# Performance work log

Measured on AMD Instinct MI355X. Metric: run time of the kernel, lower is better.

Reference implementation:

```python
import jax, jax.numpy as jnp
import numpy as np

T, H, I, E, K, L, R = 1024, 1024, 1024, 8, 2, 4, 16
N = 2 * I  # gate_up dim


def setup_inputs() -> dict:
    key = jax.random.key(0)
    ks = jax.random.split(key, 12)
    tw = jax.random.uniform(ks[1], (T, K), dtype=jnp.float32) + 0.1
    tw = tw / tw.sum(axis=-1, keepdims=True)  # routing weights sum to 1
    return {
        "hidden_states": jax.random.normal(ks[0], (T, H), dtype=jnp.float32),
        "topk_weights": tw,
        "w13": jax.random.normal(ks[2], (E, N, H), dtype=jnp.float32) * (1.0 / np.sqrt(H)),
        "w2": jax.random.normal(ks[3], (E, H, I), dtype=jnp.float32) * (1.0 / np.sqrt(I)),
        "gate_up_lora_a": jax.random.normal(ks[4], (L, E, R, H), dtype=jnp.float32) * (1.0 / np.sqrt(H)),
        "gate_up_lora_b": jax.random.normal(ks[5], (L, E, N, R), dtype=jnp.float32) * (1.0 / np.sqrt(R)),
        "down_lora_a": jax.random.normal(ks[6], (L, E, R, I), dtype=jnp.float32) * (1.0 / np.sqrt(I)),
        "down_lora_b": jax.random.normal(ks[7], (L, E, H, R), dtype=jnp.float32) * (1.0 / np.sqrt(R)),
        "scalings": jax.random.uniform(ks[8], (L,), dtype=jnp.float32) + 0.5,
        "topk_ids": jax.random.randint(ks[9], (T, K), 0, E, dtype=jnp.int32),
        "lora_indices": jax.random.randint(ks[10], (T,), 0, L, dtype=jnp.int32),
    }


def reference(hidden_states, topk_weights, w13, w2, gate_up_lora_a,
              gate_up_lora_b, down_lora_a, down_lora_b, scalings,
              topk_ids, lora_indices):
    num_tokens, hidden = hidden_states.shape
    num_experts, gate_up_dim, _ = w13.shape
    top_k = topk_ids.shape[1]
    inter = gate_up_dim // 2
    TKp = num_tokens * top_k

    e_flat = topk_ids.reshape(-1)                      # [TK] expert per dispatched pair
    l_flat = jnp.repeat(lora_indices, top_k)           # [TK] adapter per pair
    w_flat = topk_weights.reshape(-1)                  # [TK] routing weight
    x_rep = jnp.repeat(hidden_states, top_k, axis=0)   # [TK, H]

    # ---- grouped gate_up GEMM (base path): cache1[p] = x[p] @ w13[e(p)]^T ----
    cache1 = jnp.zeros((TKp, gate_up_dim), dtype=hidden_states.dtype)
    for ei in range(num_experts):  # small fixed expert count
        mask = (e_flat == ei)[:, None]
        cache1 = cache1 + jnp.where(mask, x_rep @ w13[ei].T, 0.0)

    # ---- per-expert gate_up LoRA delta, injected BEFORE activation ----
    scal = scalings[l_flat][:, None]                   # [TK, 1]
    Ag = gate_up_lora_a[l_flat, e_flat]                # [TK, R, H]
    Bg = gate_up_lora_b[l_flat, e_flat]                # [TK, N, R]
    tmp = jnp.einsum('prh,ph->pr', Ag, x_rep)
    cache1 = cache1 + jnp.einsum('pnr,pr->pn', Bg, tmp) * scal

    # ---- silu_and_mul on (base + lora) ----
    act = jax.nn.silu(cache1[:, :inter]) * cache1[:, inter:]   # [TK, I]

    # ---- grouped down GEMM (base), routed-weight applied ----
    cache3 = jnp.zeros((TKp, hidden), dtype=hidden_states.dtype)
    for ei in range(num_experts):
        mask = (e_flat == ei)[:, None]
        cache3 = cache3 + jnp.where(mask, act @ w2[ei].T, 0.0)
    cache3 = cache3 * w_flat[:, None]

    # ---- per-expert down LoRA delta (weighted by routing weight) ----
    Ad = down_lora_a[l_flat, e_flat]                   # [TK, R, I]
    Bd = down_lora_b[l_flat, e_flat]                   # [TK, H, R]
    tmpd = jnp.einsum('pri,pi->pr', Ad, act)
    cache3 = cache3 + jnp.einsum('phr,pr->ph', Bd, tmpd) * scal * w_flat[:, None]

    # ---- combine expert outputs (moe_sum over top_k slots) ----
    return cache3.reshape(num_tokens, top_k, hidden).sum(axis=1)
```

## Files before the change

kernel.cpp:

```cpp
#include <hip/hip_runtime.h>
#include <stdint.h>

#define Td 1024
#define Hd 1024
#define Id 1024
#define Ed 8
#define Kd 2
#define Ld 4
#define Rd 16
#define Nd 2048
#define TKd (Td*Kd)

typedef __bf16 bf16x8 __attribute__((ext_vector_type(8)));
typedef float f32x4 __attribute__((ext_vector_type(4)));

__device__ __forceinline__ ushort f2bf(float f) {
    uint32_t u = __builtin_bit_cast(uint32_t, f);
    return (ushort)((u + 0x7fffu + ((u >> 16) & 1u)) >> 16);
}
__device__ __forceinline__ float bf2f(ushort u) {
    uint32_t x = ((uint32_t)u) << 16;
    return __builtin_bit_cast(float, x);
}
__device__ __forceinline__ void cvt16(const float* __restrict__ s, ushort* __restrict__ d) {
    float4 a0 = *(const float4*)(s);
    float4 a1 = *(const float4*)(s + 4);
    float4 a2 = *(const float4*)(s + 8);
    float4 a3 = *(const float4*)(s + 12);
    uint4 o0, o1;
    o0.x = (uint)f2bf(a0.x) | ((uint)f2bf(a0.y) << 16);
    o0.y = (uint)f2bf(a0.z) | ((uint)f2bf(a0.w) << 16);
    o0.z = (uint)f2bf(a1.x) | ((uint)f2bf(a1.y) << 16);
    o0.w = (uint)f2bf(a1.z) | ((uint)f2bf(a1.w) << 16);
    o1.x = (uint)f2bf(a2.x) | ((uint)f2bf(a2.y) << 16);
    o1.y = (uint)f2bf(a2.z) | ((uint)f2bf(a2.w) << 16);
    o1.z = (uint)f2bf(a3.x) | ((uint)f2bf(a3.y) << 16);
    o1.w = (uint)f2bf(a3.z) | ((uint)f2bf(a3.w) << 16);
    *(uint4*)(d) = o0;
    *(uint4*)(d + 8) = o1;
}

#define GLOAD_LDS16(g, l) __builtin_amdgcn_global_load_lds( \
    (const __attribute__((address_space(1))) uint32_t*)(const void*)(g), \
    (__attribute__((address_space(3))) uint32_t*)(void*)(l), 16, 0, 0)

#define W13C 4096
#define TB 2048
#define XB 256
#define CB 384
#define ZB 1024
#define PREP_BLOCKS (W13C + TB + XB + CB + ZB + 1)

__global__ __launch_bounds__(256) void k_prep(
    const float* __restrict__ hid, const float* __restrict__ w13,
    const float* __restrict__ gb, const float* __restrict__ db,
    const float* __restrict__ ga, const float* __restrict__ sc,
    const int* __restrict__ tids, const int* __restrict__ lidx,
    ushort* __restrict__ xb, ushort* __restrict__ w13b,
    ushort* __restrict__ gbbe, ushort* __restrict__ dbbe, ushort* __restrict__ tmp1e,
    float* __restrict__ out, int* __restrict__ sorted, int* __restrict__ offs)
{
    __shared__ float tr[Rd];
    __shared__ int cnt[Ed];
    __shared__ int cur[Ed];
    const int b = blockIdx.x, tid = threadIdx.x;

    if (b < W13C) {
        size_t off = ((size_t)b * 256 + tid) * 16;
        cvt16(w13 + off, w13b + off);
    } else if (b < W13C + TB) {
        const int p = b - W13C;
        const int e = tids[p];
        const int l = lidx[p >> 1];
        const float s = sc[l];
        const int r = tid >> 4, q = tid & 15;
        const float* A = ga + (((size_t)l * Ed + e) * Rd + r) * 1024;
        const float* x = hid + (size_t)(p >> 1) * 1024;
        float sum = 0.f;
        #pragma unroll
        for (int i = 0; i < 16; ++i) {
            int h = q * 4 + 64 * i;
            float4 a = *(const float4*)(A + h);
            float4 v = *(const float4*)(x + h);
            sum += a.x * v.x + a.y * v.y + a.z * v.z + a.w * v.w;
        }
        sum += __shfl_xor(sum, 1); sum += __shfl_xor(sum, 2);
        sum += __shfl_xor(sum, 4); sum += __shfl_xor(sum, 8);
        if (q == 0) tr[r] = sum;
        __syncthreads();
        if (tid < 32) {
            int j0 = tid * 2;
            uint v = 0;
            if ((j0 >> 4) == l)
                v = (uint)f2bf(s * tr[j0 & 15]) | ((uint)f2bf(s * tr[(j0 + 1) & 15]) << 16);
            ((uint*)(tmp1e + (size_t)p * 64))[tid] = v;
        }
    } else if (b < W13C + TB + XB) {
        size_t off = ((size_t)(b - W13C - TB) * 256 + tid) * 16;
        cvt16(hid + off, xb + off);
    } else if (b < W13C + TB + XB + CB) {
        constexpr int GR = Ld * Ed * Nd;
        int i = (b - W13C - TB - XB) * 256 + tid;
        const float* src; ushort* dst;
        if (i < GR) {
            int l = i >> 14, e = (i >> 11) & 7, n = i & 2047;
            src = gb + (size_t)i * 16;
            dst = gbbe + ((size_t)(e * Nd + n)) * 64 + l * 16;
        } else {
            int j = i - GR;
            int l = j >> 13, e = (j >> 10) & 7, n = j & 1023;
            src = db + (size_t)j * 16;
            dst = dbbe + ((size_t)(e * Id + n)) * 64 + l * 16;
        }
        cvt16(src, dst);
    } else if (b < W13C + TB + XB + CB + ZB) {
        int i = (b - W13C - TB - XB - CB) * 256 + tid;
        ((float4*)out)[i] = make_float4(0.f, 0.f, 0.f, 0.f);
    } else {
        if (tid < Ed) cnt[tid] = 0;
        __syncthreads();
        int el[8];
        #pragma unroll
        for (int i = 0; i < 8; ++i) {
            el[i] = tids[tid + i * 256];
            atomicAdd(&cnt[el[i]], 1);
        }
        __syncthreads();
        if (tid == 0) {
            int s = 0;
            for (int e = 0; e < Ed; ++e) { offs[e] = s; cur[e] = s; s += cnt[e]; }
            offs[Ed] = s;
        }
        __syncthreads();
        #pragma unroll
        for (int i = 0; i < 8; ++i) {
            int pos = atomicAdd(&cur[el[i]], 1);
            sorted[pos] = tid + i * 256;
        }
    }
}

__global__ __launch_bounds__(256) void k_tmp_dn(
    const ushort* __restrict__ act, const float* __restrict__ da,
    const float* __restrict__ sc, const int* __restrict__ tids,
    const int* __restrict__ lidx, ushort* __restrict__ tmpde)
{
    const int p = blockIdx.x;
    const int e = tids[p];
    const int l = lidx[p >> 1];
    const float s = sc[l];
    const int tid = threadIdx.x;
    const int r = tid >> 4, q = tid & 15;
    const float* A = da + (((size_t)l * Ed + e) * Rd + r) * 1024;
    const ushort* x = act + (size_t)p * 1024;
    float sum = 0.f;
    #pragma unroll
    for (int i = 0; i < 8; ++i) {
        int h = q * 8 + 128 * i;
        float4 a0 = *(const float4*)(A + h);
        float4 a1 = *(const float4*)(A + h + 4);
        ushort4 v0 = *(const ushort4*)(x + h);
        ushort4 v1 = *(const ushort4*)(x + h + 4);
        sum += a0.x * bf2f(v0.x) + a0.y * bf2f(v0.y) + a0.z * bf2f(v0.z) + a0.w * bf2f(v0.w)
             + a1.x * bf2f(v1.x) + a1.y * bf2f(v1.y) + a1.z * bf2f(v1.z) + a1.w * bf2f(v1.w);
    }
    sum += __shfl_xor(sum, 1); sum += __shfl_xor(sum, 2);
    sum += __shfl_xor(sum, 4); sum += __shfl_xor(sum, 8);
    __shared__ float tr[Rd];
    if (q == 0) tr[r] = sum;
    __syncthreads();
    if (tid < 32) {
        int j0 = tid * 2;
        uint v = 0;
        if ((j0 >> 4) == l)
            v = (uint)f2bf(s * tr[j0 & 15]) | ((uint)f2bf(s * tr[(j0 + 1) & 15]) << 16);
        ((uint*)(tmpde + (size_t)p * 64))[tid] = v;
    }
}

#define GUB 512
#define W2C 2048

__global__ __launch_bounds__(256) void k_gemm_gu(
    const ushort* __restrict__ xb, const ushort* __restrict__ w13b,
    const ushort* __restrict__ tmp1e, const ushort* __restrict__ gbbe,
    const float* __restrict__ w2, ushort* __restrict__ w2b,
    ushort* __restrict__ act, const int* __restrict__ sorted,
    const int* __restrict__ offs)
{
    __shared__ ushort As[128][32];
    __shared__ ushort Bs[128][32];
    const int tid = threadIdx.x;

    if (blockIdx.x >= GUB) {
        size_t off = ((size_t)(blockIdx.x - GUB) * 256 + tid) * 16;
        cvt16(w2 + off, w2b + off);
        return;
    }

    const int lane = tid & 63, wave = tid >> 6;
    const int wr = wave >> 1, wc = wave & 1;
    const int fr = lane & 15, fk = (lane >> 4) * 8;

    int off[Ed + 1];
    #pragma unroll
    for (int e = 0; e <= Ed; ++e) off[e] = offs[e];
    int mt[Ed]; int tot = 0;
    #pragma unroll
    for (int e = 0; e < Ed; ++e) {
        mt[e] = (off[e + 1] - off[e] + 127) / 128;
        tot += mt[e] * 16;
    }

    for (int tau = blockIdx.x; tau < tot; tau += GUB) {
        int t = tau, e = 0;
        while (t >= mt[e] * 16) { t -= mt[e] * 16; ++e; }
        const int m0 = off[e] + (t >> 4) * 128;
        const int mend = off[e + 1];
        const int n0 = (t & 15) * 64;

        const ushort *asrc[2], *aesrc[2], *bsrc[2], *besrc[2];
        #pragma unroll
        for (int r = 0; r < 2; ++r) {
            int c = r * 256 + tid;
            int row = c >> 2, kc = c & 3;
            int aIdx = m0 + row; if (aIdx > mend - 1) aIdx = mend - 1;
            int p = sorted[aIdx];
            asrc[r]  = xb + (size_t)(p >> 1) * 1024 + kc * 8;
            aesrc[r] = tmp1e + (size_t)p * 64 + kc * 8;
            int grow = (row < 64) ? (n0 + row) : (1024 + n0 + row - 64);
            bsrc[r]  = w13b + ((size_t)e * Nd + grow) * 1024 + kc * 8;
            besrc[r] = gbbe + ((size_t)e * Nd + grow) * 64 + kc * 8;
        }

        f32x4 ag[4][2] = {}, au[4][2] = {};
        auto step = [&]() {
            bf16x8 af[4], bg[2], bu[2];
            #pragma unroll
            for (int mi = 0; mi < 4; ++mi)
                af[mi] = *(const bf16x8*)(&As[wr * 64 + mi * 16 + fr][fk]);
            #pragma unroll
            for (int ni = 0; ni < 2; ++ni) {
                bg[ni] = *(const bf16x8*)(&Bs[wc * 32 + ni * 16 + fr][fk]);
                bu[ni] = *(const bf16x8*)(&Bs[64 + wc * 32 + ni * 16 + fr][fk]);
            }
            #pragma unroll
            for (int mi = 0; mi < 4; ++mi)
                #pragma unroll
                for (int ni = 0; ni < 2; ++ni) {
                    ag[mi][ni] = __builtin_amdgcn_mfma_f32_16x16x32_bf16(af[mi], bg[ni], ag[mi][ni], 0, 0, 0);
                    au[mi][ni] = __builtin_amdgcn_mfma_f32_16x16x32_bf16(af[mi], bu[ni], au[mi][ni], 0, 0, 0);
                }
        };

        for (int k0 = 0; k0 < 1024; k0 += 32) {
            #pragma unroll
            for (int r = 0; r < 2; ++r) {
                GLOAD_LDS16(asrc[r] + k0, (char*)&As[0][0] + (r * 256 + wave * 64) * 16);
                GLOAD_LDS16(bsrc[r] + k0, (char*)&Bs[0][0] + (r * 256 + wave * 64) * 16);
            }
            __syncthreads();
            step();
            __syncthreads();
        }
        #pragma unroll
        for (int es = 0; es < 2; ++es) {
            #pragma unroll
            for (int r = 0; r < 2; ++r) {
                GLOAD_LDS16(aesrc[r] + es * 32, (char*)&As[0][0] + (r * 256 + wave * 64) * 16);
                GLOAD_LDS16(besrc[r] + es * 32, (char*)&Bs[0][0] + (r * 256 + wave * 64) * 16);
            }
            __syncthreads();
            step();
            __syncthreads();
        }

        const int rb = wr * 64 + (lane >> 4) * 4;
        #pragma unroll
        for (int mi = 0; mi < 4; ++mi) {
            #pragma unroll
            for (int j = 0; j < 4; ++j) {
                int sidx = m0 + rb + mi * 16 + j;
                if (sidx < mend) {
                    int p = sorted[sidx];
                    ushort* ar = act + (size_t)p * 1024 + n0 + wc * 32;
                    #pragma unroll
                    for (int ni = 0; ni < 2; ++ni) {
                        float g = ag[mi][ni][j], u = au[mi][ni][j];
                        float v = g / (1.f + __expf(-g)) * u;
                        ar[ni * 16 + fr] = f2bf(v);
                    }
                }
            }
        }
    }
}

__global__ __launch_bounds__(256) void k_gemm_dn(
    const ushort* __restrict__ act, const ushort* __restrict__ w2b,
    const ushort* __restrict__ tmpde, const ushort* __restrict__ dbbe,
    const float* __restrict__ tw, float* __restrict__ out,
    const int* __restrict__ sorted, const int* __restrict__ offs)
{
    __shared__ ushort As[128][32];
    __shared__ ushort Bs[64][32];
    const int tid = threadIdx.x, lane = tid & 63, wave = tid >> 6;
    const int wr = wave >> 1, wc = wave & 1;
    const int fr = lane & 15, fk = (lane >> 4) * 8;

    int off[Ed + 1];
    #pragma unroll
    for (int e = 0; e <= Ed; ++e) off[e] = offs[e];
    int mt[Ed]; int tot = 0;
    #pragma unroll
    for (int e = 0; e < Ed; ++e) {
        mt[e] = (off[e + 1] - off[e] + 127) / 128;
        tot += mt[e] * 16;
    }

    for (int tau = blockIdx.x; tau < tot; tau += gridDim.x) {
        int t = tau, e = 0;
        while (t >= mt[e] * 16) { t -= mt[e] * 16; ++e; }
        const int m0 = off[e] + (t >> 4) * 128;
        const int mend = off[e + 1];
        const int n0 = (t & 15) * 64;

        const ushort *asrc[2], *aesrc[2];
        #pragma unroll
        for (int r = 0; r < 2; ++r) {
            int c = r * 256 + tid;
            int row = c >> 2, kc = c & 3;
            int aIdx = m0 + row; if (aIdx > mend - 1) aIdx = mend - 1;
            int p = sorted[aIdx];
            asrc[r]  = act + (size_t)p * 1024 + kc * 8;
            aesrc[r] = tmpde + (size_t)p * 64 + kc * 8;
        }
        const ushort *bsrc, *besrc;
        {
            int row = tid >> 2, kc = tid & 3;
            bsrc  = w2b + ((size_t)e * Hd + n0 + row) * 1024 + kc * 8;
            besrc = dbbe + ((size_t)e * Hd + n0 + row) * 64 + kc * 8;
        }

        f32x4 acc[4][2] = {};
        auto step = [&]() {
            bf16x8 af[4], bv[2];
            #pragma unroll
            for (int mi = 0; mi < 4; ++mi)
                af[mi] = *(const bf16x8*)(&As[wr * 64 + mi * 16 + fr][fk]);
            #pragma unroll
            for (int ni = 0; ni < 2; ++ni)
                bv[ni] = *(const bf16x8*)(&Bs[wc * 32 + ni * 16 + fr][fk]);
            #pragma unroll
            for (int mi = 0; mi < 4; ++mi)
                #pragma unroll
                for (int ni = 0; ni < 2; ++ni)
                    acc[mi][ni] = __builtin_amdgcn_mfma_f32_16x16x32_bf16(af[mi], bv[ni], acc[mi][ni], 0, 0, 0);
        };

        for (int k0 = 0; k0 < 1024; k0 += 32) {
            #pragma unroll
            for (int r = 0; r < 2; ++r)
                GLOAD_LDS16(asrc[r] + k0, (char*)&As[0][0] + (r * 256 + wave * 64) * 16);
            GLOAD_LDS16(bsrc + k0, (char*)&Bs[0][0] + (wave * 64) * 16);
            __syncthreads();
            step();
            __syncthreads();
        }
        #pragma unroll
        for (int es = 0; es < 2; ++es) {
            #pragma unroll
            for (int r = 0; r < 2; ++r)
                GLOAD_LDS16(aesrc[r] + es * 32, (char*)&As[0][0] + (r * 256 + wave * 64) * 16);
            GLOAD_LDS16(besrc + es * 32, (char*)&Bs[0][0] + (wave * 64) * 16);
            __syncthreads();
            step();
            __syncthreads();
        }

        const int rb = wr * 64 + (lane >> 4) * 4;
        #pragma unroll
        for (int mi = 0; mi < 4; ++mi) {
            #pragma unroll
            for (int j = 0; j < 4; ++j) {
                int sidx = m0 + rb + mi * 16 + j;
                if (sidx < mend) {
                    int p = sorted[sidx];
                    float w = tw[p];
                    float* orow = out + (size_t)(p >> 1) * 1024 + n0 + wc * 32;
                    #pragma unroll
                    for (int ni = 0; ni < 2; ++ni)
                        atomicAdd(&orow[ni * 16 + fr], w * acc[mi][ni][j]);
                }
            }
        }
    }
}

extern "C" void kernel_launch(void* const* d_in, const int* in_sizes, int n_in,
                              void* d_out, int out_size, void* d_ws, size_t ws_size,
                              hipStream_t stream) {
    const float* hid  = (const float*)d_in[0];
    const float* tw   = (const float*)d_in[1];
    const float* w13  = (const float*)d_in[2];
    const float* w2   = (const float*)d_in[3];
    const float* ga   = (const float*)d_in[4];
    const float* gb   = (const float*)d_in[5];
    const float* da   = (const float*)d_in[6];
    const float* db   = (const float*)d_in[7];
    const float* sc   = (const float*)d_in[8];
    const int*   tids = (const int*)d_in[9];
    const int*   lidx = (const int*)d_in[10];
    float* out = (float*)d_out;

    char* ws = (char*)d_ws;
    ushort* xb     = (ushort*)(ws);
    ushort* w13b   = (ushort*)(ws + (2ull  << 20));
    ushort* w2b    = (ushort*)(ws + (34ull << 20));
    ushort* gbbe   = (ushort*)(ws + (50ull << 20));
    ushort* dbbe   = (ushort*)(ws + (52ull << 20));
    ushort* tmp1e  = (ushort*)(ws + (53ull << 20));
    ushort* tmpde  = (ushort*)(ws + (53ull << 20) + (256u << 10));
    ushort* act    = (ushort*)(ws + (54ull << 20));
    int*    sorted = (int*)(ws + (58ull << 20));
    int*    offs   = (int*)(ws + (58ull << 20) + TKd * 4);

    k_prep<<<PREP_BLOCKS, 256, 0, stream>>>(hid, w13, gb, db, ga, sc, tids, lidx,
                                            xb, w13b, gbbe, dbbe, tmp1e, out, sorted, offs);
    k_gemm_gu<<<GUB + W2C, 256, 0, stream>>>(xb, w13b, tmp1e, gbbe, w2, w2b, act, sorted, offs);
    k_tmp_dn<<<TKd, 256, 0, stream>>>(act, da, sc, tids, lidx, tmpde);
    k_gemm_dn<<<512, 256, 0, stream>>>(act, w2b, tmpde, dbbe, tw, out, sorted, offs);
}
```

Baseline: 103.1 us.

## Double-buffer LDS tiles in gate_up and down grouped GEMMs

Both grouped GEMM kernels now keep two LDS buffers for A and B tiles. The global-to-LDS load of the next K-slice, including the LoRA extension slices, is issued before the MFMA work on the current slice. This leaves one barrier per iteration instead of two. The aim is to hide global load latency behind compute, at the cost of doubled LDS use, which may lower occupancy. A barrier is still needed before the loads land, and correctness depends on the async LDS loads completing by the next barrier.

```diff
diff --git a/kernel.cpp b/kernel.cpp
--- a/kernel.cpp
+++ b/kernel.cpp
@@ -188,8 +188,8 @@
     ushort* __restrict__ act, const int* __restrict__ sorted,
     const int* __restrict__ offs)
 {
-    __shared__ ushort As[128][32];
-    __shared__ ushort Bs[128][32];
+    __shared__ ushort As[2][128][32];
+    __shared__ ushort Bs[2][128][32];
     const int tid = threadIdx.x;
 
     if (blockIdx.x >= GUB) {
@@ -234,15 +234,32 @@
         }
 
         f32x4 ag[4][2] = {}, au[4][2] = {};
-        auto step = [&]() {
+        auto stage = [&](int s, int b) {
+            if (s < 32) {
+                int k0 = s * 32;
+                #pragma unroll
+                for (int r = 0; r < 2; ++r) {
+                    GLOAD_LDS16(asrc[r] + k0, (char*)&As[b][0][0] + (r * 256 + wave * 64) * 16);
+                    GLOAD_LDS16(bsrc[r] + k0, (char*)&Bs[b][0][0] + (r * 256 + wave * 64) * 16);
+                }
+            } else {
+                int k0 = (s - 32) * 32;
+                #pragma unroll
+                for (int r = 0; r < 2; ++r) {
+                    GLOAD_LDS16(aesrc[r] + k0, (char*)&As[b][0][0] + (r * 256 + wave * 64) * 16);
+                    GLOAD_LDS16(besrc[r] + k0, (char*)&Bs[b][0][0] + (r * 256 + wave * 64) * 16);
+                }
+            }
+        };
+        auto step = [&](int b) {
             bf16x8 af[4], bg[2], bu[2];
             #pragma unroll
             for (int mi = 0; mi < 4; ++mi)
-                af[mi] = *(const bf16x8*)(&As[wr * 64 + mi * 16 + fr][fk]);
+                af[mi] = *(const bf16x8*)(&As[b][wr * 64 + mi * 16 + fr][fk]);
             #pragma unroll
             for (int ni = 0; ni < 2; ++ni) {
-                bg[ni] = *(const bf16x8*)(&Bs[wc * 32 + ni * 16 + fr][fk]);
-                bu[ni] = *(const bf16x8*)(&Bs[64 + wc * 32 + ni * 16 + fr][fk]);
+                bg[ni] = *(const bf16x8*)(&Bs[b][wc * 32 + ni * 16 + fr][fk]);
+                bu[ni] = *(const bf16x8*)(&Bs[b][64 + wc * 32 + ni * 16 + fr][fk]);
             }
             #pragma unroll
             for (int mi = 0; mi < 4; ++mi)
@@ -253,26 +270,14 @@
                 }
         };
 
-        for (int k0 = 0; k0 < 1024; k0 += 32) {
-            #pragma unroll
-            for (int r = 0; r < 2; ++r) {
-                GLOAD_LDS16(asrc[r] + k0, (char*)&As[0][0] + (r * 256 + wave * 64) * 16);
-                GLOAD_LDS16(bsrc[r] + k0, (char*)&Bs[0][0] + (r * 256 + wave * 64) * 16);
-            }
+        stage(0, 0);
+        __syncthreads();
+        int buf = 0;
+        for (int s = 0; s < 34; ++s) {
+            if (s < 33) stage(s + 1, buf ^ 1);
+            step(buf);
             __syncthreads();
-            step();
-            __syncthreads();
-        }
-        #pragma unroll
-        for (int es = 0; es < 2; ++es) {
-            #pragma unroll
-            for (int r = 0; r < 2; ++r) {
-                GLOAD_LDS16(aesrc[r] + es * 32, (char*)&As[0][0] + (r * 256 + wave * 64) * 16);
-                GLOAD_LDS16(besrc[r] + es * 32, (char*)&Bs[0][0] + (r * 256 + wave * 64) * 16);
-            }
-            __syncthreads();
-            step();
-            __syncthreads();
+            buf ^= 1;
         }
 
         const int rb = wr * 64 + (lane >> 4) * 4;
@@ -302,8 +307,8 @@
     const float* __restrict__ tw, float* __restrict__ out,
     const int* __restrict__ sorted, const int* __restrict__ offs)
 {
-    __shared__ ushort As[128][32];
-    __shared__ ushort Bs[64][32];
+    __shared__ ushort As[2][128][32];
+    __shared__ ushort Bs[2][64][32];
     const int tid = threadIdx.x, lane = tid & 63, wave = tid >> 6;
     const int wr = wave >> 1, wc = wave & 1;
     const int fr = lane & 15, fk = (lane >> 4) * 8;
@@ -343,14 +348,29 @@
         }
 
         f32x4 acc[4][2] = {};
-        auto step = [&]() {
+        auto stage = [&](int s, int b) {
+            if (s < 32) {
+                int k0 = s * 32;
+                #pragma unroll
+                for (int r = 0; r < 2; ++r)
+                    GLOAD_LDS16(asrc[r] + k0, (char*)&As[b][0][0] + (r * 256 + wave * 64) * 16);
+                GLOAD_LDS16(bsrc + k0, (char*)&Bs[b][0][0] + (wave * 64) * 16);
+            } else {
+                int k0 = (s - 32) * 32;
+                #pragma unroll
+                for (int r = 0; r < 2; ++r)
+                    GLOAD_LDS16(aesrc[r] + k0, (char*)&As[b][0][0] + (r * 256 + wave * 64) * 16);
+                GLOAD_LDS16(besrc + k0, (char*)&Bs[b][0][0] + (wave * 64) * 16);
+            }
+        };
+        auto step = [&](int b) {
             bf16x8 af[4], bv[2];
             #pragma unroll
             for (int mi = 0; mi < 4; ++mi)
-                af[mi] = *(const bf16x8*)(&As[wr * 64 + mi * 16 + fr][fk]);
+                af[mi] = *(const bf16x8*)(&As[b][wr * 64 + mi * 16 + fr][fk]);
             #pragma unroll
             for (int ni = 0; ni < 2; ++ni)
-                bv[ni] = *(const bf16x8*)(&Bs[wc * 32 + ni * 16 + fr][fk]);
+                bv[ni] = *(const bf16x8*)(&Bs[b][wc * 32 + ni * 16 + fr][fk]);
             #pragma unroll
             for (int mi = 0; mi < 4; ++mi)
                 #pragma unroll
@@ -358,24 +378,14 @@
                     acc[mi][ni] = __builtin_amdgcn_mfma_f32_16x16x32_bf16(af[mi], bv[ni], acc[mi][ni], 0, 0, 0);
         };
 
-        for (int k0 = 0; k0 < 1024; k0 += 32) {
-            #pragma unroll
-            for (int r = 0; r < 2; ++r)
-                GLOAD_LDS16(asrc[r] + k0, (char*)&As[0][0] + (r * 256 + wave * 64) * 16);
-            GLOAD_LDS16(bsrc + k0, (char*)&Bs[0][0] + (wave * 64) * 16);
+        stage(0, 0);
+        __syncthreads();
+        int buf = 0;
+        for (int s = 0; s < 34; ++s) {
+            if (s < 33) stage(s + 1, buf ^ 1);
+            step(buf);
             __syncthreads();
-            step();
-            __syncthreads();
-        }
-        #pragma unroll
-        for (int es = 0; es < 2; ++es) {
-            #pragma unroll
-            for (int r = 0; r < 2; ++r)
-                GLOAD_LDS16(aesrc[r] + es * 32, (char*)&As[0][0] + (r * 256 + wave * 64) * 16);
-            GLOAD_LDS16(besrc + es * 32, (char*)&Bs[0][0] + (wave * 64) * 16);
-            __syncthreads();
-            step();
-            __syncthreads();
+            buf ^= 1;
         }
 
         const int rb = wr * 64 + (lane >> 4) * 4;
```

Measured after the change: 111.0 us. 7.7% more time.

## Fuse w13 fp32-to-bf16 conversion into gate-up GEMM with double-buffered LDS

Applied to the files above, without the earlier changes.

The separate pass that converts w13 to bf16 is dropped. The gate-up GEMM now loads fp32 w13 directly, converts it in registers and writes it into a double-buffered shared-memory tile, so the next tile's loads overlap the current MFMA step. The w2 conversion moves into the prep kernel. Both GEMMs shrink the M tile from 128 to 64 rows and launch 1024 blocks for more parallelism. The cost is that each GEMM block re-reads fp32 weights, which is twice the bytes per load, and the smaller tiles give less weight reuse per block.

```diff
diff --git a/kernel.cpp b/kernel.cpp
--- a/kernel.cpp
+++ b/kernel.cpp
@@ -21,6 +21,12 @@
 __device__ __forceinline__ float bf2f(ushort u) {
     uint32_t x = ((uint32_t)u) << 16;
     return __builtin_bit_cast(float, x);
+}
+__device__ __forceinline__ bf16x8 pack8(float4 a, float4 b) {
+    bf16x8 r;
+    r[0] = (__bf16)a.x; r[1] = (__bf16)a.y; r[2] = (__bf16)a.z; r[3] = (__bf16)a.w;
+    r[4] = (__bf16)b.x; r[5] = (__bf16)b.y; r[6] = (__bf16)b.z; r[7] = (__bf16)b.w;
+    return r;
 }
 __device__ __forceinline__ void cvt16(const float* __restrict__ s, ushort* __restrict__ d) {
     float4 a0 = *(const float4*)(s);
@@ -44,19 +50,19 @@
     (const __attribute__((address_space(1))) uint32_t*)(const void*)(g), \
     (__attribute__((address_space(3))) uint32_t*)(void*)(l), 16, 0, 0)
 
-#define W13C 4096
+#define W2C 2048
 #define TB 2048
 #define XB 256
 #define CB 384
 #define ZB 1024
-#define PREP_BLOCKS (W13C + TB + XB + CB + ZB + 1)
+#define PREP_BLOCKS (W2C + TB + XB + CB + ZB + 1)
 
 __global__ __launch_bounds__(256) void k_prep(
-    const float* __restrict__ hid, const float* __restrict__ w13,
+    const float* __restrict__ hid, const float* __restrict__ w2,
     const float* __restrict__ gb, const float* __restrict__ db,
     const float* __restrict__ ga, const float* __restrict__ sc,
     const int* __restrict__ tids, const int* __restrict__ lidx,
-    ushort* __restrict__ xb, ushort* __restrict__ w13b,
+    ushort* __restrict__ xb, ushort* __restrict__ w2b,
     ushort* __restrict__ gbbe, ushort* __restrict__ dbbe, ushort* __restrict__ tmp1e,
     float* __restrict__ out, int* __restrict__ sorted, int* __restrict__ offs)
 {
@@ -65,11 +71,11 @@
     __shared__ int cur[Ed];
     const int b = blockIdx.x, tid = threadIdx.x;
 
-    if (b < W13C) {
+    if (b < W2C) {
         size_t off = ((size_t)b * 256 + tid) * 16;
-        cvt16(w13 + off, w13b + off);
-    } else if (b < W13C + TB) {
-        const int p = b - W13C;
+        cvt16(w2 + off, w2b + off);
+    } else if (b < W2C + TB) {
+        const int p = b - W2C;
         const int e = tids[p];
         const int l = lidx[p >> 1];
         const float s = sc[l];
@@ -95,12 +101,12 @@
                 v = (uint)f2bf(s * tr[j0 & 15]) | ((uint)f2bf(s * tr[(j0 + 1) & 15]) << 16);
             ((uint*)(tmp1e + (size_t)p * 64))[tid] = v;
         }
-    } else if (b < W13C + TB + XB) {
-        size_t off = ((size_t)(b - W13C - TB) * 256 + tid) * 16;
+    } else if (b < W2C + TB + XB) {
+        size_t off = ((size_t)(b - W2C - TB) * 256 + tid) * 16;
         cvt16(hid + off, xb + off);
-    } else if (b < W13C + TB + XB + CB) {
+    } else if (b < W2C + TB + XB + CB) {
         constexpr int GR = Ld * Ed * Nd;
-        int i = (b - W13C - TB - XB) * 256 + tid;
+        int i = (b - W2C - TB - XB) * 256 + tid;
         const float* src; ushort* dst;
         if (i < GR) {
             int l = i >> 14, e = (i >> 11) & 7, n = i & 2047;
@@ -113,8 +119,8 @@
             dst = dbbe + ((size_t)(e * Id + n)) * 64 + l * 16;
         }
         cvt16(src, dst);
-    } else if (b < W13C + TB + XB + CB + ZB) {
-        int i = (b - W13C - TB - XB - CB) * 256 + tid;
+    } else if (b < W2C + TB + XB + CB + ZB) {
+        int i = (b - W2C - TB - XB - CB) * 256 + tid;
         ((float4*)out)[i] = make_float4(0.f, 0.f, 0.f, 0.f);
     } else {
         if (tid < Ed) cnt[tid] = 0;
@@ -178,27 +184,15 @@
     }
 }
 
-#define GUB 512
-#define W2C 2048
-
 __global__ __launch_bounds__(256) void k_gemm_gu(
-    const ushort* __restrict__ xb, const ushort* __restrict__ w13b,
+    const ushort* __restrict__ xb, const float* __restrict__ w13,
     const ushort* __restrict__ tmp1e, const ushort* __restrict__ gbbe,
-    const float* __restrict__ w2, ushort* __restrict__ w2b,
     ushort* __restrict__ act, const int* __restrict__ sorted,
     const int* __restrict__ offs)
 {
-    __shared__ ushort As[128][32];
-    __shared__ ushort Bs[128][32];
-    const int tid = threadIdx.x;
-
-    if (blockIdx.x >= GUB) {
-        size_t off = ((size_t)(blockIdx.x - GUB) * 256 + tid) * 16;
-        cvt16(w2 + off, w2b + off);
-        return;
-    }
-
-    const int lane = tid & 63, wave = tid >> 6;
+    __shared__ ushort As[2][64][32];
+    __shared__ ushort Bs[2][128][32];
+    const int tid = threadIdx.x, lane = tid & 63, wave = tid >> 6;
     const int wr = wave >> 1, wc = wave & 1;
     const int fr = lane & 15, fk = (lane >> 4) * 8;
 
@@ -208,44 +202,49 @@
     int mt[Ed]; int tot = 0;
     #pragma unroll
     for (int e = 0; e < Ed; ++e) {
-        mt[e] = (off[e + 1] - off[e] + 127) / 128;
+        mt[e] = (off[e + 1] - off[e] + 63) / 64;
         tot += mt[e] * 16;
     }
 
-    for (int tau = blockIdx.x; tau < tot; tau += GUB) {
+    for (int tau = blockIdx.x; tau < tot; tau += gridDim.x) {
         int t = tau, e = 0;
         while (t >= mt[e] * 16) { t -= mt[e] * 16; ++e; }
-        const int m0 = off[e] + (t >> 4) * 128;
+        const int m0 = off[e] + (t >> 4) * 64;
         const int mend = off[e + 1];
         const int n0 = (t & 15) * 64;
 
-        const ushort *asrc[2], *aesrc[2], *bsrc[2], *besrc[2];
+        const ushort *asrc, *aesrc;
+        {
+            int aIdx = m0 + (tid >> 2); if (aIdx > mend - 1) aIdx = mend - 1;
+            int p = sorted[aIdx];
+            asrc  = xb + (size_t)(p >> 1) * 1024 + (tid & 3) * 8;
+            aesrc = tmp1e + (size_t)p * 64 + (tid & 3) * 8;
+        }
+        const int brow = tid >> 1, bhalf = tid & 1;
+        const int bg_row = (brow < 64) ? (n0 + brow) : (1024 + n0 + brow - 64);
+        const float* bsrc = w13 + ((size_t)e * Nd + bg_row) * 1024 + bhalf * 16;
+        const ushort* besrc[2];
         #pragma unroll
         for (int r = 0; r < 2; ++r) {
             int c = r * 256 + tid;
             int row = c >> 2, kc = c & 3;
-            int aIdx = m0 + row; if (aIdx > mend - 1) aIdx = mend - 1;
-            int p = sorted[aIdx];
-            asrc[r]  = xb + (size_t)(p >> 1) * 1024 + kc * 8;
-            aesrc[r] = tmp1e + (size_t)p * 64 + kc * 8;
             int grow = (row < 64) ? (n0 + row) : (1024 + n0 + row - 64);
-            bsrc[r]  = w13b + ((size_t)e * Nd + grow) * 1024 + kc * 8;
             besrc[r] = gbbe + ((size_t)e * Nd + grow) * 64 + kc * 8;
         }
 
-        f32x4 ag[4][2] = {}, au[4][2] = {};
-        auto step = [&]() {
-            bf16x8 af[4], bg[2], bu[2];
-            #pragma unroll
-            for (int mi = 0; mi < 4; ++mi)
-                af[mi] = *(const bf16x8*)(&As[wr * 64 + mi * 16 + fr][fk]);
+        f32x4 ag[2][2] = {}, au[2][2] = {};
+        auto step = [&](int b) {
+            bf16x8 af[2], bg[2], bu[2];
+            #pragma unroll
+            for (int mi = 0; mi < 2; ++mi)
+                af[mi] = *(const bf16x8*)(&As[b][wr * 32 + mi * 16 + fr][fk]);
             #pragma unroll
             for (int ni = 0; ni < 2; ++ni) {
-                bg[ni] = *(const bf16x8*)(&Bs[wc * 32 + ni * 16 + fr][fk]);
-                bu[ni] = *(const bf16x8*)(&Bs[64 + wc * 32 + ni * 16 + fr][fk]);
+                bg[ni] = *(const bf16x8*)(&Bs[b][wc * 32 + ni * 16 + fr][fk]);
+                bu[ni] = *(const bf16x8*)(&Bs[b][64 + wc * 32 + ni * 16 + fr][fk]);
             }
             #pragma unroll
-            for (int mi = 0; mi < 4; ++mi)
+            for (int mi = 0; mi < 2; ++mi)
                 #pragma unroll
                 for (int ni = 0; ni < 2; ++ni) {
                     ag[mi][ni] = __builtin_amdgcn_mfma_f32_16x16x32_bf16(af[mi], bg[ni], ag[mi][ni], 0, 0, 0);
@@ -253,31 +252,47 @@
                 }
         };
 
-        for (int k0 = 0; k0 < 1024; k0 += 32) {
-            #pragma unroll
-            for (int r = 0; r < 2; ++r) {
-                GLOAD_LDS16(asrc[r] + k0, (char*)&As[0][0] + (r * 256 + wave * 64) * 16);
-                GLOAD_LDS16(bsrc[r] + k0, (char*)&Bs[0][0] + (r * 256 + wave * 64) * 16);
-            }
-            __syncthreads();
-            step();
-            __syncthreads();
-        }
+        GLOAD_LDS16(asrc, (char*)&As[0][0][0] + (wave * 64) * 16);
+        {
+            float4 y0 = *(const float4*)(bsrc);
+            float4 y1 = *(const float4*)(bsrc + 4);
+            float4 y2 = *(const float4*)(bsrc + 8);
+            float4 y3 = *(const float4*)(bsrc + 12);
+            *(bf16x8*)(&Bs[0][brow][bhalf * 16])     = pack8(y0, y1);
+            *(bf16x8*)(&Bs[0][brow][bhalf * 16 + 8]) = pack8(y2, y3);
+        }
+        __syncthreads();
+
+        int buf = 0;
+        for (int k0 = 32; k0 < 1024; k0 += 32) {
+            GLOAD_LDS16(asrc + k0, (char*)&As[buf ^ 1][0][0] + (wave * 64) * 16);
+            float4 y0 = *(const float4*)(bsrc + k0);
+            float4 y1 = *(const float4*)(bsrc + k0 + 4);
+            float4 y2 = *(const float4*)(bsrc + k0 + 8);
+            float4 y3 = *(const float4*)(bsrc + k0 + 12);
+
+            step(buf);
+
+            *(bf16x8*)(&Bs[buf ^ 1][brow][bhalf * 16])     = pack8(y0, y1);
+            *(bf16x8*)(&Bs[buf ^ 1][brow][bhalf * 16 + 8]) = pack8(y2, y3);
+            __syncthreads();
+            buf ^= 1;
+        }
+        step(buf);
+
         #pragma unroll
         for (int es = 0; es < 2; ++es) {
-            #pragma unroll
-            for (int r = 0; r < 2; ++r) {
-                GLOAD_LDS16(aesrc[r] + es * 32, (char*)&As[0][0] + (r * 256 + wave * 64) * 16);
-                GLOAD_LDS16(besrc[r] + es * 32, (char*)&Bs[0][0] + (r * 256 + wave * 64) * 16);
-            }
-            __syncthreads();
-            step();
-            __syncthreads();
-        }
-
-        const int rb = wr * 64 + (lane >> 4) * 4;
-        #pragma unroll
-        for (int mi = 0; mi < 4; ++mi) {
+            GLOAD_LDS16(aesrc + es * 32, (char*)&As[es][0][0] + (wave * 64) * 16);
+            #pragma unroll
+            for (int r = 0; r < 2; ++r)
+                GLOAD_LDS16(besrc[r] + es * 32, (char*)&Bs[es][0][0] + (r * 256 + wave * 64) * 16);
+            __syncthreads();
+            step(es);
+        }
+
+        const int rb = wr * 32 + (lane >> 4) * 4;
+        #pragma unroll
+        for (int mi = 0; mi < 2; ++mi) {
             #pragma unroll
             for (int j = 0; j < 4; ++j) {
                 int sidx = m0 + rb + mi * 16 + j;
@@ -293,6 +308,7 @@
                 }
             }
         }
+        __syncthreads();
     }
 }
 
@@ -302,7 +318,7 @@
     const float* __restrict__ tw, float* __restrict__ out,
     const int* __restrict__ sorted, const int* __restrict__ offs)
 {
-    __shared__ ushort As[128][32];
+    __shared__ ushort As[64][32];
     __shared__ ushort Bs[64][32];
     const int tid = threadIdx.x, lane = tid & 63, wave = tid >> 6;
     const int wr = wave >> 1, wc = wave & 1;
@@ -314,54 +330,46 @@
     int mt[Ed]; int tot = 0;
     #pragma unroll
     for (int e = 0; e < Ed; ++e) {
-        mt[e] = (off[e + 1] - off[e] + 127) / 128;
+        mt[e] = (off[e + 1] - off[e] + 63) / 64;
         tot += mt[e] * 16;
     }
 
     for (int tau = blockIdx.x; tau < tot; tau += gridDim.x) {
         int t = tau, e = 0;
         while (t >= mt[e] * 16) { t -= mt[e] * 16; ++e; }
-        const int m0 = off[e] + (t >> 4) * 128;
+        const int m0 = off[e] + (t >> 4) * 64;
         const int mend = off[e + 1];
         const int n0 = (t & 15) * 64;
 
-        const ushort *asrc[2], *aesrc[2];
-        #pragma unroll
-        for (int r = 0; r < 2; ++r) {
-            int c = r * 256 + tid;
-            int row = c >> 2, kc = c & 3;
-            int aIdx = m0 + row; if (aIdx > mend - 1) aIdx = mend - 1;
+        const ushort *asrc, *aesrc, *bsrc, *besrc;
+        {
+            int aIdx = m0 + (tid >> 2); if (aIdx > mend - 1) aIdx = mend - 1;
             int p = sorted[aIdx];
-            asrc[r]  = act + (size_t)p * 1024 + kc * 8;
-            aesrc[r] = tmpde + (size_t)p * 64 + kc * 8;
-        }
-        const ushort *bsrc, *besrc;
-        {
+            asrc  = act + (size_t)p * 1024 + (tid & 3) * 8;
+            aesrc = tmpde + (size_t)p * 64 + (tid & 3) * 8;
             int row = tid >> 2, kc = tid & 3;
             bsrc  = w2b + ((size_t)e * Hd + n0 + row) * 1024 + kc * 8;
             besrc = dbbe + ((size_t)e * Hd + n0 + row) * 64 + kc * 8;
         }
 
-        f32x4 acc[4][2] = {};
+        f32x4 acc[2][2] = {};
         auto step = [&]() {
-            bf16x8 af[4], bv[2];
-            #pragma unroll
-            for (int mi = 0; mi < 4; ++mi)
-                af[mi] = *(const bf16x8*)(&As[wr * 64 + mi * 16 + fr][fk]);
+            bf16x8 af[2], bv[2];
+            #pragma unroll
+            for (int mi = 0; mi < 2; ++mi)
+                af[mi] = *(const bf16x8*)(&As[wr * 32 + mi * 16 + fr][fk]);
             #pragma unroll
             for (int ni = 0; ni < 2; ++ni)
                 bv[ni] = *(const bf16x8*)(&Bs[wc * 32 + ni * 16 + fr][fk]);
             #pragma unroll
-            for (int mi = 0; mi < 4; ++mi)
+            for (int mi = 0; mi < 2; ++mi)
                 #pragma unroll
                 for (int ni = 0; ni < 2; ++ni)
                     acc[mi][ni] = __builtin_amdgcn_mfma_f32_16x16x32_bf16(af[mi], bv[ni], acc[mi][ni], 0, 0, 0);
         };
 
         for (int k0 = 0; k0 < 1024; k0 += 32) {
-            #pragma unroll
-            for (int r = 0; r < 2; ++r)
-                GLOAD_LDS16(asrc[r] + k0, (char*)&As[0][0] + (r * 256 + wave * 64) * 16);
+            GLOAD_LDS16(asrc + k0, (char*)&As[0][0] + (wave * 64) * 16);
             GLOAD_LDS16(bsrc + k0, (char*)&Bs[0][0] + (wave * 64) * 16);
             __syncthreads();
             step();
@@ -369,18 +377,16 @@
         }
         #pragma unroll
         for (int es = 0; es < 2; ++es) {
-            #pragma unroll
-            for (int r = 0; r < 2; ++r)
-                GLOAD_LDS16(aesrc[r] + es * 32, (char*)&As[0][0] + (r * 256 + wave * 64) * 16);
+            GLOAD_LDS16(aesrc + es * 32, (char*)&As[0][0] + (wave * 64) * 16);
             GLOAD_LDS16(besrc + es * 32, (char*)&Bs[0][0] + (wave * 64) * 16);
             __syncthreads();
             step();
             __syncthreads();
         }
 
-        const int rb = wr * 64 + (lane >> 4) * 4;
-        #pragma unroll
-        for (int mi = 0; mi < 4; ++mi) {
+        const int rb = wr * 32 + (lane >> 4) * 4;
+        #pragma unroll
+        for (int mi = 0; mi < 2; ++mi) {
             #pragma unroll
             for (int j = 0; j < 4; ++j) {
                 int sidx = m0 + rb + mi * 16 + j;
@@ -415,19 +421,18 @@
 
     char* ws = (char*)d_ws;
     ushort* xb     = (ushort*)(ws);
-    ushort* w13b   = (ushort*)(ws + (2ull  << 20));
-    ushort* w2b    = (ushort*)(ws + (34ull << 20));
-    ushort* gbbe   = (ushort*)(ws + (50ull << 20));
-    ushort* dbbe   = (ushort*)(ws + (52ull << 20));
-    ushort* tmp1e  = (ushort*)(ws + (53ull << 20));
-    ushort* tmpde  = (ushort*)(ws + (53ull << 20) + (256u << 10));
-    ushort* act    = (ushort*)(ws + (54ull << 20));
-    int*    sorted = (int*)(ws + (58ull << 20));
-    int*    offs   = (int*)(ws + (58ull << 20) + TKd * 4);
-
-    k_prep<<<PREP_BLOCKS, 256, 0, stream>>>(hid, w13, gb, db, ga, sc, tids, lidx,
-                                            xb, w13b, gbbe, dbbe, tmp1e, out, sorted, offs);
-    k_gemm_gu<<<GUB + W2C, 256, 0, stream>>>(xb, w13b, tmp1e, gbbe, w2, w2b, act, sorted, offs);
+    ushort* w2b    = (ushort*)(ws + (2ull  << 20));
+    ushort* gbbe   = (ushort*)(ws + (18ull << 20));
+    ushort* dbbe   = (ushort*)(ws + (20ull << 20));
+    ushort* tmp1e  = (ushort*)(ws + (21ull << 20));
+    ushort* tmpde  = (ushort*)(ws + (21ull << 20) + (256u << 10));
+    ushort* act    = (ushort*)(ws + (22ull << 20));
+    int*    sorted = (int*)(ws + (26ull << 20));
+    int*    offs   = (int*)(ws + (26ull << 20) + TKd * 4);
+
+    k_prep<<<PREP_BLOCKS, 256, 0, stream>>>(hid, w2, gb, db, ga, sc, tids, lidx,
+                                            xb, w2b, gbbe, dbbe, tmp1e, out, sorted, offs);
+    k_gemm_gu<<<1024, 256, 0, stream>>>(xb, w13, tmp1e, gbbe, act, sorted, offs);
     k_tmp_dn<<<TKd, 256, 0, stream>>>(act, da, sc, tids, lidx, tmpde);
-    k_gemm_dn<<<512, 256, 0, stream>>>(act, w2b, tmpde, dbbe, tw, out, sorted, offs);
-}
+    k_gemm_dn<<<1024, 256, 0, stream>>>(act, w2b, tmpde, dbbe, tw, out, sorted, offs);
+}
```

Result: faster. 92.93 us (-9.9%).
